# Performance work log

Measured on AMD Instinct MI355X. Metric: run time of the kernel, lower is better.

The kernel has to match this reference:

```python
import jax, jax.numpy as jnp
import numpy as np

D_MODEL = 2048
H_TOTAL = 32
D_HEAD = D_MODEL // H_TOTAL  # 64
H_ACTIVE = 4
ROPE_BASE = 10000.0


def _apply_rope(t, cos, sin):
    # t: [B, H, T, DH]; cos/sin: [T, DH//2]; interleaved pair rotation
    t1 = t[..., 0::2]
    t2 = t[..., 1::2]
    r1 = t1 * cos - t2 * sin
    r2 = t1 * sin + t2 * cos
    return jnp.stack([r1, r2], axis=-1).reshape(t.shape)


def setup_inputs() -> dict:
    key = jax.random.key(0)
    ks = jax.random.split(key, 4)
    x = jax.random.normal(ks[0], (4, 1024, D_MODEL), dtype=jnp.float32)
    w_router = jax.random.normal(ks[1], (D_MODEL, H_TOTAL), dtype=jnp.float32) * 0.02
    w_qkv = jax.random.normal(ks[2], (D_MODEL, 3 * D_MODEL), dtype=jnp.float32) * 0.02
    w_out = jax.random.normal(ks[3], (D_MODEL, D_MODEL), dtype=jnp.float32) * 0.02
    return {"x": x, "w_router": w_router, "w_qkv": w_qkv, "w_out": w_out}


def reference(x, w_router, w_qkv, w_out):
    B, T, _ = x.shape
    # --- SwitchRouter: per-token probabilities over heads ---
    probs = jax.nn.softmax(x @ w_router, axis=-1)            # [B, T, H]
    # top-h_active heads per token (dense-math equivalent of sparse dispatch)
    _, top_idx = jax.lax.top_k(probs, H_ACTIVE)              # [B, T, HA]
    mask = jnp.sum(jax.nn.one_hot(top_idx, H_TOTAL, dtype=x.dtype), axis=-2)  # [B, T, H]
    gate = probs * mask                                      # router-scored gate

    # --- QKV projection ---
    qkv = x @ w_qkv                                          # [B, T, 3D]
    q, k, v = jnp.split(qkv, 3, axis=-1)
    def to_heads(t):
        return t.reshape(B, T, H_TOTAL, D_HEAD).transpose(0, 2, 1, 3)  # [B, H, T, DH]
    q, k, v = to_heads(q), to_heads(k), to_heads(v)

    # --- RoPE ---
    inv_freq = 1.0 / (ROPE_BASE ** (jnp.arange(0, D_HEAD, 2, dtype=jnp.float32) / D_HEAD))
    ang = jnp.arange(T, dtype=jnp.float32)[:, None] * inv_freq[None, :]  # [T, DH/2]
    cos, sin = jnp.cos(ang), jnp.sin(ang)
    q = _apply_rope(q, cos, sin)
    k = _apply_rope(k, cos, sin)

    # --- causal SDPA ---
    scores = jnp.einsum('bhqd,bhkd->bhqk', q, k) / np.float32(np.sqrt(D_HEAD))
    causal = jnp.tril(jnp.ones((T, T), dtype=bool))
    scores = jnp.where(causal, scores, jnp.finfo(scores.dtype).min)
    attn = jax.nn.softmax(scores, axis=-1)
    out = jnp.einsum('bhqk,bhkd->bhqd', attn, v)             # [B, H, T, DH]

    # --- gate: only active heads contribute (scatter-back equivalent) ---
    out = out * gate.transpose(0, 2, 1)[..., None]           # [B, H, T, DH]
    out = out.transpose(0, 2, 1, 3).reshape(B, T, D_MODEL)
    return out @ w_out
```

## Files before the change

### kernel.cpp

```cpp
#include <hip/hip_runtime.h>
#include <hip/hip_bf16.h>
#include <stdint.h>
#include <stddef.h>

typedef __attribute__((ext_vector_type(8))) short bf16x8;
typedef __attribute__((ext_vector_type(8))) unsigned short u16x8;
typedef __attribute__((ext_vector_type(4))) float f32x4;
typedef __attribute__((ext_vector_type(16))) float f32x16;

#define TT 1024

__device__ __forceinline__ unsigned short f2bf(float f){
  unsigned u = __builtin_bit_cast(unsigned, f);
  unsigned r = 0x7fffu + ((u >> 16) & 1u);
  return (unsigned short)((u + r) >> 16);
}
__device__ __forceinline__ float bf2f(unsigned short s){
  unsigned u = ((unsigned)s) << 16;
  return __builtin_bit_cast(float, u);
}
__device__ __forceinline__ void gload16(const unsigned short* g, unsigned short* l){
  __builtin_amdgcn_global_load_lds(
      (const __attribute__((address_space(1))) void*)g,
      (__attribute__((address_space(3))) void*)l, 16, 0, 0);
}

__global__ void transpose_cast_kernel(const float* __restrict__ in, unsigned short* __restrict__ out,
                                      int R, int C){
  __shared__ float tile[32][33];
  int c0 = blockIdx.x * 32, r0 = blockIdx.y * 32;
  for (int i = threadIdx.y; i < 32; i += 8)
    tile[i][threadIdx.x] = in[(size_t)(r0 + i) * C + c0 + threadIdx.x];
  __syncthreads();
  for (int i = threadIdx.y; i < 32; i += 8)
    out[(size_t)(c0 + i) * R + r0 + threadIdx.x] = f2bf(tile[threadIdx.x][i]);
}

__global__ void rope_table_kernel(float* __restrict__ tab){
  int idx = blockIdx.x * 256 + threadIdx.x;
  int pos = idx >> 5, i = idx & 31;
  float freq = powf(10000.0f, -(float)i / 32.0f);
  float ang = (float)pos * freq;
  tab[idx * 2]     = cosf(ang);
  tab[idx * 2 + 1] = sinf(ang);
}

__global__ __launch_bounds__(256) void prep_kernel(const float* __restrict__ x,
                                                   const float* __restrict__ wr,
                                                   unsigned short* __restrict__ x_bf,
                                                   float* __restrict__ gate){
  __shared__ float xc[8 * 256];
  __shared__ float red[8 * 8 * 32];
  const int tid = threadIdx.x;
  const int tok0 = blockIdx.x * 8;
  const int p = tid >> 5, h = tid & 31;
  float acc[8] = {0.f,0.f,0.f,0.f,0.f,0.f,0.f,0.f};

  for (int kb = 0; kb < 8; kb++){
    __syncthreads();
    {
      int tok = tid >> 5, e = (tid & 31) * 8;
      const float* xp = x + (size_t)(tok0 + tok) * 2048 + kb * 256 + e;
      float4 v0 = *(const float4*)xp, v1 = *(const float4*)(xp + 4);
      float vals[8] = {v0.x, v0.y, v0.z, v0.w, v1.x, v1.y, v1.z, v1.w};
      u16x8 ob;
      #pragma unroll
      for (int jj = 0; jj < 8; jj++) ob[jj] = f2bf(vals[jj]);
      *(u16x8*)(x_bf + (size_t)(tok0 + tok) * 2048 + kb * 256 + e) = ob;
      #pragma unroll
      for (int jj = 0; jj < 8; jj++) xc[tok * 256 + e + jj] = vals[jj];
    }
    __syncthreads();
    const float* wp = wr + (size_t)(kb * 256 + p * 32) * 32 + h;
    #pragma unroll 4
    for (int j = 0; j < 32; j++){
      float wv = wp[j * 32];
      #pragma unroll
      for (int tok = 0; tok < 8; tok++)
        acc[tok] += xc[tok * 256 + p * 32 + j] * wv;
    }
  }
  #pragma unroll
  for (int tok = 0; tok < 8; tok++) red[(p * 8 + tok) * 32 + h] = acc[tok];
  __syncthreads();
  {
    int lane = tid & 63;
    int tok = (tid >> 6) * 2 + (lane >> 5);
    int hh = lane & 31;
    float logit = 0.f;
    #pragma unroll
    for (int pp = 0; pp < 8; pp++) logit += red[(pp * 8 + tok) * 32 + hh];
    float m = logit;
    #pragma unroll
    for (int s = 16; s >= 1; s >>= 1) m = fmaxf(m, __shfl_xor(m, s));
    float e = __expf(logit - m);
    float sum = e;
    #pragma unroll
    for (int s = 16; s >= 1; s >>= 1) sum += __shfl_xor(sum, s);
    float prob = e / sum;
    float v = logit; int sel = 0;
    #pragma unroll
    for (int rr2 = 0; rr2 < 4; rr2++){
      float bv = v; int bi = hh;
      #pragma unroll
      for (int s = 16; s >= 1; s >>= 1){
        float ov = __shfl_xor(bv, s); int oi = __shfl_xor(bi, s);
        if (ov > bv || (ov == bv && oi < bi)) { bv = ov; bi = oi; }
      }
      if (hh == bi) { sel = 1; v = -3.4e38f; }
    }
    gate[(size_t)(tok0 + tok) * 32 + hh] = sel ? prob : 0.f;
  }
}

__global__ void compact_kernel(const float* __restrict__ gate, int* __restrict__ idx,
                               int* __restrict__ counts){
  int bh = blockIdx.x;
  int b = bh >> 5, h = bh & 31;
  int lane = threadIdx.x;
  int base = 0;
  for (int c = 0; c < 16; c++){
    int t = c * 64 + lane;
    bool act = gate[(size_t)(b * TT + t) * 32 + h] != 0.f;
    unsigned long long mask = __ballot(act);
    int pos = base + __popcll(mask & ((1ull << lane) - 1ull));
    if (act) idx[bh * TT + pos] = t;
    base += __popcll(mask);
  }
  if (lane == 0) counts[bh] = base;
}

#define MFMA32(a, b, c) __builtin_amdgcn_mfma_f32_32x32x16_bf16((a), (b), (c), 0, 0, 0)

template<int EPI>
__global__ __launch_bounds__(256, 1) void gemm32(const unsigned short* __restrict__ A,
                                                 const unsigned short* __restrict__ Bt,
                                                 float* __restrict__ Cf,
                                                 unsigned short* __restrict__ qk,
                                                 unsigned short* __restrict__ vt,
                                                 const float* __restrict__ tab,
                                                 int N, int K, int nbm){
  extern __shared__ unsigned short smem[];

  const int nblk = gridDim.x;
  const int raw = blockIdx.x;
  const int tile = (raw & 7) * (nblk >> 3) + (raw >> 3);
  const int bn = tile / nbm, bm = tile % nbm;

  const int tid = threadIdx.x, lane = tid & 63, wid = tid >> 6;
  const int wrow = wid >> 1, wcol = wid & 1;
  const int l31 = lane & 31, hi = lane >> 5;
  const int X = (l31 & 7) << 4;

  const unsigned short* gA[8];
  const unsigned short* gB[4];
  #pragma unroll
  for (int p = 0; p < 8; p++){
    int L = tid * 16 + p * 4096;
    int r = L >> 7, c = (L & 127) ^ ((r & 7) << 4);
    gA[p] = A + (size_t)(bm * 256 + r) * K + (c >> 1);
  }
  #pragma unroll
  for (int p = 0; p < 4; p++){
    int L = tid * 16 + p * 4096;
    int r = L >> 7, c = (L & 127) ^ ((r & 7) << 4);
    gB[p] = Bt + (size_t)(bn * 128 + r) * K + (c >> 1);
  }

  auto stageA0 = [&](int tt){
    unsigned short* b = smem + (tt % 3) * 24576;
    size_t ko = (size_t)tt * 64;
    gload16(gA[0] + ko, b + tid * 8);
    gload16(gA[1] + ko, b + tid * 8 + 2048);
    gload16(gA[2] + ko, b + tid * 8 + 4096);
    gload16(gA[3] + ko, b + tid * 8 + 6144);
  };
  auto stageA1 = [&](int tt){
    unsigned short* b = smem + (tt % 3) * 24576;
    size_t ko = (size_t)tt * 64;
    gload16(gA[4] + ko, b + tid * 8 + 8192);
    gload16(gA[5] + ko, b + tid * 8 + 10240);
    gload16(gA[6] + ko, b + tid * 8 + 12288);
    gload16(gA[7] + ko, b + tid * 8 + 14336);
  };
  auto stageB = [&](int tt){
    unsigned short* b = smem + (tt % 3) * 24576 + 16384;
    size_t ko = (size_t)tt * 64;
    gload16(gB[0] + ko, b + tid * 8);
    gload16(gB[1] + ko, b + tid * 8 + 2048);
    gload16(gB[2] + ko, b + tid * 8 + 4096);
    gload16(gB[3] + ko, b + tid * 8 + 6144);
  };

  f32x16 acc[4][2];
  #pragma unroll
  for (int i = 0; i < 4; i++)
    #pragma unroll
    for (int j = 0; j < 2; j++) acc[i][j] = f32x16{0,0,0,0,0,0,0,0,0,0,0,0,0,0,0,0};

  const int NT = K >> 6;
  stageA0(0); stageA1(0); stageB(0);
  stageA0(1); stageA1(1); stageB(1);

  const int arow = (wrow * 128 + l31) * 64;
  const int brow = 16384 + (wcol * 64 + l31) * 64;

  for (int t = 0; t < NT; ++t){
    if (t < NT - 1) asm volatile("s_waitcnt vmcnt(12)" ::: "memory");
    else            asm volatile("s_waitcnt vmcnt(0)" ::: "memory");
    __builtin_amdgcn_s_barrier();
    __builtin_amdgcn_sched_barrier(0);
    const unsigned short* bs = smem + (t % 3) * 24576;
    const bool st = (t + 2 < NT);
    #pragma unroll
    for (int ks = 0; ks < 4; ks++){
      const int kp = ((ks * 32 + hi * 16) ^ X) >> 1;
      bf16x8 a0 = *(const bf16x8*)(bs + arow +        kp);
      bf16x8 a1 = *(const bf16x8*)(bs + arow + 2048 + kp);
      bf16x8 a2 = *(const bf16x8*)(bs + arow + 4096 + kp);
      bf16x8 a3 = *(const bf16x8*)(bs + arow + 6144 + kp);
      bf16x8 b0 = *(const bf16x8*)(bs + brow +        kp);
      bf16x8 b1 = *(const bf16x8*)(bs + brow + 2048 + kp);
      if (st && ks == 0) stageA0(t + 2);
      if (st && ks == 1) stageA1(t + 2);
      if (st && ks == 2) stageB(t + 2);
      acc[0][0] = MFMA32(a0, b0, acc[0][0]); acc[0][1] = MFMA32(a0, b1, acc[0][1]);
      acc[1][0] = MFMA32(a1, b0, acc[1][0]); acc[1][1] = MFMA32(a1, b1, acc[1][1]);
      acc[2][0] = MFMA32(a2, b0, acc[2][0]); acc[2][1] = MFMA32(a2, b1, acc[2][1]);
      acc[3][0] = MFMA32(a3, b0, acc[3][0]); acc[3][1] = MFMA32(a3, b1, acc[3][1]);
    }
  }

  if (EPI == 1){
    if (bn < 32){
      #pragma unroll
      for (int i = 0; i < 4; i++){
        #pragma unroll
        for (int j = 0; j < 2; j++){
          int col = bn * 128 + wcol * 64 + j * 32 + l31;
          int ii = (col & 63) >> 1;
          #pragma unroll
          for (int g = 0; g < 4; g++){
            #pragma unroll
            for (int rr = 0; rr < 4; rr++){
              int row = bm * 256 + wrow * 128 + i * 32 + g * 8 + hi * 4 + rr;
              int pos = row & (TT - 1);
              const float* tp = tab + ((size_t)pos * 32 + ii) * 2;
              float c = tp[0], s = tp[1];
              float val = acc[i][j][g * 4 + rr];
              float pv = __shfl_xor(val, 1);
              float res = (lane & 1) ? (pv * s + val * c) : (val * c - pv * s);
              qk[(size_t)row * 4096 + col] = f2bf(res);
            }
          }
        }
      }
    } else {
      #pragma unroll
      for (int i = 0; i < 4; i++){
        #pragma unroll
        for (int j = 0; j < 2; j++){
          int vcol = bn * 128 + wcol * 64 + j * 32 + l31 - 4096;
          int hh = vcol >> 6, d = vcol & 63;
          int row0 = bm * 256 + wrow * 128 + i * 32 + hi * 4;
          int b = row0 >> 10, t0 = row0 & (TT - 1);
          #pragma unroll
          for (int g = 0; g < 4; g++){
            ushort4 pk;
            pk.x = f2bf(acc[i][j][g * 4 + 0]); pk.y = f2bf(acc[i][j][g * 4 + 1]);
            pk.z = f2bf(acc[i][j][g * 4 + 2]); pk.w = f2bf(acc[i][j][g * 4 + 3]);
            *(ushort4*)(vt + ((size_t)((b * 32 + hh) * 64 + d)) * TT + t0 + g * 8) = pk;
          }
        }
      }
    }
  } else {
    #pragma unroll
    for (int i = 0; i < 4; i++){
      #pragma unroll
      for (int j = 0; j < 2; j++){
        int col = bn * 128 + wcol * 64 + j * 32 + l31;
        #pragma unroll
        for (int g = 0; g < 4; g++){
          #pragma unroll
          for (int rr = 0; rr < 4; rr++){
            size_t row = (size_t)(bm * 256 + wrow * 128 + i * 32 + g * 8 + hi * 4 + rr);
            Cf[row * N + col] = acc[i][j][g * 4 + rr];
          }
        }
      }
    }
  }
}

#define MFMA_B16(a, b, c) __builtin_amdgcn_mfma_f32_16x16x32_bf16((a), (b), (c), 0, 0, 0)
__global__ __launch_bounds__(256) void attn_sparse_kernel(const unsigned short* __restrict__ qk,
                                                          const unsigned short* __restrict__ vt,
                                                          const float* __restrict__ gate,
                                                          const int* __restrict__ idx,
                                                          const int* __restrict__ counts,
                                                          unsigned short* __restrict__ attn_out){
  __shared__ unsigned short Ks[64 * 64];
  __shared__ unsigned short Vs[64 * 64];
  __shared__ unsigned short Ps[4][16 * 64];
  const int bh = blockIdx.x, qt = blockIdx.y;
  const int count = counts[bh];
  if (qt * 64 >= count) return;
  const int b = bh >> 5, h = bh & 31;
  const int tid = threadIdx.x, lane = tid & 63, w = tid >> 6;
  const int li = lane & 15, lg = lane >> 4;
  const int* myidx = idx + bh * TT + qt * 64;
  const int nvalid = min(64, count - qt * 64);
  const int qmax = myidx[nvalid - 1];

  int qi[4];
  #pragma unroll
  for (int r = 0; r < 4; r++){
    int s = w * 16 + lg * 4 + r;
    qi[r] = (s < nvalid) ? myidx[s] : -1;
  }
  int qrow = (w * 16 + li < nvalid) ? myidx[w * 16 + li] : 0;
  bf16x8 qf0, qf1;
  {
    const unsigned short* qp = qk + (size_t)(b * TT + qrow) * 4096 + h * 64;
    qf0 = *(const bf16x8*)(qp + lg * 8);
    qf1 = *(const bf16x8*)(qp + 32 + lg * 8);
  }
  f32x4 o[4];
  #pragma unroll
  for (int i = 0; i < 4; i++) o[i] = f32x4{0.f, 0.f, 0.f, 0.f};
  float m_run[4], l_run[4];
  #pragma unroll
  for (int r = 0; r < 4; r++){ m_run[r] = -1e30f; l_run[r] = 0.f; }

  const int nkt = (qmax >> 6) + 1;
  for (int kt = 0; kt < nkt; kt++){
    const int kb = kt * 64;
    #pragma unroll
    for (int s2 = 0; s2 < 2; s2++){
      int s = s2 * 256 + tid;
      int r = s >> 3, c = (s & 7) * 8;
      gload16(qk + (size_t)(b * TT + kb + r) * 4096 + 2048 + h * 64 + c, &Ks[s * 8]);
      gload16(vt + (size_t)(bh * 64 + r) * TT + kb + c, &Vs[s * 8]);
    }
    __syncthreads();

    f32x4 s4[4];
    #pragma unroll
    for (int ni = 0; ni < 4; ni++){
      bf16x8 k0 = *(const bf16x8*)(&Ks[(ni * 16 + li) * 64 + lg * 8]);
      bf16x8 k1 = *(const bf16x8*)(&Ks[(ni * 16 + li) * 64 + 32 + lg * 8]);
      f32x4 t = f32x4{0.f, 0.f, 0.f, 0.f};
      t = MFMA_B16(qf0, k0, t);
      t = MFMA_B16(qf1, k1, t);
      s4[ni] = t;
    }
    float mt[4];
    #pragma unroll
    for (int r = 0; r < 4; r++) mt[r] = -1e30f;
    #pragma unroll
    for (int ni = 0; ni < 4; ni++){
      int kidx = kb + ni * 16 + li;
      #pragma unroll
      for (int r = 0; r < 4; r++){
        float val = s4[ni][r] * 0.125f;
        val = (kidx <= qi[r]) ? val : -1e30f;
        s4[ni][r] = val;
        mt[r] = fmaxf(mt[r], val);
      }
    }
    #pragma unroll
    for (int r = 0; r < 4; r++){
      #pragma unroll
      for (int sh = 8; sh >= 1; sh >>= 1) mt[r] = fmaxf(mt[r], __shfl_xor(mt[r], sh));
      float mnew = fmaxf(m_run[r], mt[r]);
      float corr = __expf(m_run[r] - mnew);
      m_run[r] = mnew;
      l_run[r] *= corr;
      #pragma unroll
      for (int j = 0; j < 4; j++) o[j][r] *= corr;
    }
    float rs[4] = {0.f, 0.f, 0.f, 0.f};
    #pragma unroll
    for (int ni = 0; ni < 4; ni++)
      #pragma unroll
      for (int r = 0; r < 4; r++){
        float p = __expf(s4[ni][r] - m_run[r]);
        s4[ni][r] = p;
        rs[r] += p;
      }
    #pragma unroll
    for (int r = 0; r < 4; r++){
      #pragma unroll
      for (int sh = 8; sh >= 1; sh >>= 1) rs[r] += __shfl_xor(rs[r], sh);
      l_run[r] += rs[r];
    }
    #pragma unroll
    for (int ni = 0; ni < 4; ni++)
      #pragma unroll
      for (int r = 0; r < 4; r++)
        Ps[w][(lg * 4 + r) * 64 + ni * 16 + li] = f2bf(s4[ni][r]);
    #pragma unroll
    for (int ks = 0; ks < 2; ks++){
      bf16x8 pa = *(const bf16x8*)(&Ps[w][li * 64 + ks * 32 + lg * 8]);
      #pragma unroll
      for (int ni = 0; ni < 4; ni++){
        bf16x8 vb = *(const bf16x8*)(&Vs[(ni * 16 + li) * 64 + ks * 32 + lg * 8]);
        o[ni] = MFMA_B16(pa, vb, o[ni]);
      }
    }
    __syncthreads();
  }
  #pragma unroll
  for (int r = 0; r < 4; r++){
    if (qi[r] < 0) continue;
    float g = gate[(size_t)(b * TT + qi[r]) * 32 + h];
    float inv = g / l_run[r];
    #pragma unroll
    for (int ni = 0; ni < 4; ni++)
      attn_out[(size_t)(b * TT + qi[r]) * 2048 + h * 64 + ni * 16 + li] = f2bf(o[ni][r] * inv);
  }
}

extern "C" void kernel_launch(void* const* d_in, const int* in_sizes, int n_in,
                              void* d_out, int out_size, void* d_ws, size_t ws_size,
                              hipStream_t stream){
  const float* x        = (const float*)d_in[0];
  const float* w_router = (const float*)d_in[1];
  const float* w_qkv    = (const float*)d_in[2];
  const float* w_out    = (const float*)d_in[3];
  float* out = (float*)d_out;
  char* ws = (char*)d_ws;

  unsigned short* qk    = (unsigned short*)(ws);
  unsigned short* vt    = (unsigned short*)(ws + 33554432);
  unsigned short* x_bf  = (unsigned short*)(ws + 50331648);
  unsigned short* wqkvT = (unsigned short*)(ws + 67108864);
  unsigned short* woutT = (unsigned short*)(ws + 92274688);
  float* gate           = (float*)(ws + 100663296);
  float* tab            = (float*)(ws + 101187584);
  unsigned short* attn  = x_bf;
  int* idx              = (int*)(ws + 67108864);
  int* counts           = (int*)(ws + 67633152);

  constexpr int GEMM_LDS = 147456;
  (void)hipFuncSetAttribute(reinterpret_cast<const void*>(&gemm32<1>),
                            hipFuncAttributeMaxDynamicSharedMemorySize, GEMM_LDS);
  (void)hipFuncSetAttribute(reinterpret_cast<const void*>(&gemm32<0>),
                            hipFuncAttributeMaxDynamicSharedMemorySize, GEMM_LDS);

  hipLaunchKernelGGL(transpose_cast_kernel, dim3(192, 64), dim3(32, 8), 0, stream, w_qkv, wqkvT, 2048, 6144);
  hipLaunchKernelGGL(transpose_cast_kernel, dim3(64, 64), dim3(32, 8), 0, stream, w_out, woutT, 2048, 2048);
  hipLaunchKernelGGL(rope_table_kernel, dim3(128), dim3(256), 0, stream, tab);
  hipLaunchKernelGGL(prep_kernel, dim3(512), dim3(256), 0, stream, x, w_router, x_bf, gate);
  hipLaunchKernelGGL((gemm32<1>), dim3(768), dim3(256), GEMM_LDS, stream,
                     x_bf, wqkvT, (float*)nullptr, qk, vt, tab, 6144, 2048, 16);
  hipLaunchKernelGGL(compact_kernel, dim3(128), dim3(64), 0, stream, gate, idx, counts);
  (void)hipMemsetAsync(attn, 0, (size_t)4096 * 2048 * 2, stream);
  hipLaunchKernelGGL(attn_sparse_kernel, dim3(128, 16), dim3(256), 0, stream, qk, vt, gate, idx, counts, attn);
  hipLaunchKernelGGL((gemm32<0>), dim3(256), dim3(256), GEMM_LDS, stream,
                     attn, woutT, out, (unsigned short*)nullptr, (unsigned short*)nullptr,
                     (const float*)nullptr, 2048, 2048, 16);
}
```

Baseline: 270.1 us.

## Compute Q projection only for router-selected token-head pairs via sparse gather GEMM

The dense QKV GEMM now produces only K and V (4096 columns). A new gathered qgemm_kernel computes Q only for the top-4 active heads of each token, with RoPE applied in its epilogue. To support this, prep_kernel emits per-token head lists and compact_kernel runs before the GEMM, storing a slot index alongside each token. This cuts the dense GEMM work by a third, since only 4 of 32 heads need Q. The cost is a gather-based GEMM with uncoalesced row loads that has no LDS staging and splits K across waves with an LDS reduction.

```diff
diff --git a/kernel.cpp b/kernel.cpp
--- a/kernel.cpp
+++ b/kernel.cpp
@@ -24,6 +24,9 @@
       (const __attribute__((address_space(1))) void*)g,
       (__attribute__((address_space(3))) void*)l, 16, 0, 0);
 }
+
+#define MFMA32(a, b, c) __builtin_amdgcn_mfma_f32_32x32x16_bf16((a), (b), (c), 0, 0, 0)
+#define MFMA_B16(a, b, c) __builtin_amdgcn_mfma_f32_16x16x32_bf16((a), (b), (c), 0, 0, 0)
 
 __global__ void transpose_cast_kernel(const float* __restrict__ in, unsigned short* __restrict__ out,
                                       int R, int C){
@@ -48,7 +51,8 @@
 __global__ __launch_bounds__(256) void prep_kernel(const float* __restrict__ x,
                                                    const float* __restrict__ wr,
                                                    unsigned short* __restrict__ x_bf,
-                                                   float* __restrict__ gate){
+                                                   float* __restrict__ gate,
+                                                   unsigned char* __restrict__ heads4){
   __shared__ float xc[8 * 256];
   __shared__ float red[8 * 8 * 32];
   const int tid = threadIdx.x;
@@ -110,38 +114,121 @@
       if (hh == bi) { sel = 1; v = -3.4e38f; }
     }
     gate[(size_t)(tok0 + tok) * 32 + hh] = sel ? prob : 0.f;
-  }
-}
-
-__global__ void compact_kernel(const float* __restrict__ gate, int* __restrict__ idx,
-                               int* __restrict__ counts){
+    unsigned long long bal = __ballot(sel != 0);
+    unsigned selmask = (unsigned)(bal >> ((lane >> 5) * 32));
+    if (sel){
+      int r = __popc(selmask & ((1u << hh) - 1u));
+      heads4[(size_t)(tok0 + tok) * 4 + r] = (unsigned char)hh;
+    }
+  }
+}
+
+__global__ void compact_kernel(const unsigned char* __restrict__ heads4,
+                               unsigned short* __restrict__ idx, int* __restrict__ counts){
   int bh = blockIdx.x;
   int b = bh >> 5, h = bh & 31;
   int lane = threadIdx.x;
   int base = 0;
   for (int c = 0; c < 16; c++){
     int t = c * 64 + lane;
-    bool act = gate[(size_t)(b * TT + t) * 32 + h] != 0.f;
+    unsigned u = ((const unsigned*)heads4)[b * 1024 + t];
+    int r = -1;
+    if (((u      ) & 255) == (unsigned)h) r = 0;
+    else if (((u >>  8) & 255) == (unsigned)h) r = 1;
+    else if (((u >> 16) & 255) == (unsigned)h) r = 2;
+    else if (((u >> 24) & 255) == (unsigned)h) r = 3;
+    bool act = (r >= 0);
     unsigned long long mask = __ballot(act);
     int pos = base + __popcll(mask & ((1ull << lane) - 1ull));
-    if (act) idx[bh * TT + pos] = t;
+    if (act) idx[bh * 1024 + pos] = (unsigned short)(t | (r << 10));
     base += __popcll(mask);
   }
   if (lane == 0) counts[bh] = base;
 }
 
-#define MFMA32(a, b, c) __builtin_amdgcn_mfma_f32_32x32x16_bf16((a), (b), (c), 0, 0, 0)
+__global__ __launch_bounds__(256) void qgemm_kernel(const unsigned short* __restrict__ x_bf,
+                                                    const unsigned short* __restrict__ wqkvT,
+                                                    const unsigned short* __restrict__ idx,
+                                                    const int* __restrict__ counts,
+                                                    const float* __restrict__ tab,
+                                                    unsigned short* __restrict__ qact){
+  __shared__ float red[4][64][64];
+  const int bh = blockIdx.x, qt = blockIdx.y;
+  const int count = counts[bh];
+  if (qt * 64 >= count) return;
+  const int b = bh >> 5, h = bh & 31;
+  const int tid = threadIdx.x, lane = tid & 63, w = tid >> 6;
+  const int li = lane & 15, lg = lane >> 4;
+  const int nvalid = min(64, count - qt * 64);
+  const unsigned short* myidx = idx + bh * 1024 + qt * 64;
+
+  int atok[4];
+  #pragma unroll
+  for (int ai = 0; ai < 4; ai++){
+    int s = ai * 16 + li;
+    atok[ai] = (s < nvalid) ? (myidx[s] & 1023) : 0;
+  }
+  const unsigned short* Bbase = wqkvT + (size_t)(h * 64) * 2048;
+
+  f32x4 acc[4][4];
+  #pragma unroll
+  for (int i = 0; i < 4; i++)
+    #pragma unroll
+    for (int j = 0; j < 4; j++) acc[i][j] = f32x4{0.f, 0.f, 0.f, 0.f};
+
+  const int k0w = w * 512;
+  #pragma unroll 2
+  for (int ks = 0; ks < 16; ks++){
+    int k0 = k0w + ks * 32 + lg * 8;
+    bf16x8 af[4], bw[4];
+    #pragma unroll
+    for (int ai = 0; ai < 4; ai++)
+      af[ai] = *(const bf16x8*)(x_bf + (size_t)(b * 1024 + atok[ai]) * 2048 + k0);
+    #pragma unroll
+    for (int ni = 0; ni < 4; ni++)
+      bw[ni] = *(const bf16x8*)(Bbase + (size_t)(ni * 16 + li) * 2048 + k0);
+    #pragma unroll
+    for (int ai = 0; ai < 4; ai++)
+      #pragma unroll
+      for (int ni = 0; ni < 4; ni++)
+        acc[ai][ni] = MFMA_B16(af[ai], bw[ni], acc[ai][ni]);
+  }
+  #pragma unroll
+  for (int ai = 0; ai < 4; ai++)
+    #pragma unroll
+    for (int ni = 0; ni < 4; ni++)
+      #pragma unroll
+      for (int rr = 0; rr < 4; rr++)
+        red[w][ai * 16 + lg * 4 + rr][ni * 16 + li] = acc[ai][ni][rr];
+  __syncthreads();
+
+  int q = tid >> 2, dbase = (tid & 3) * 16;
+  if (q < nvalid){
+    int e = myidx[q];
+    int tok = e & 1023, r = e >> 10;
+    unsigned short* op = qact + ((size_t)((b << 10) + tok) * 4 + r) * 64;
+    const float* tp = tab + ((size_t)tok * 32 + (dbase >> 1)) * 2;
+    #pragma unroll
+    for (int p = 0; p < 8; p++){
+      int d0 = dbase + 2 * p;
+      float v0 = red[0][q][d0] + red[1][q][d0] + red[2][q][d0] + red[3][q][d0];
+      float v1 = red[0][q][d0 + 1] + red[1][q][d0 + 1] + red[2][q][d0 + 1] + red[3][q][d0 + 1];
+      float c = tp[2 * p], s = tp[2 * p + 1];
+      op[d0]     = f2bf(v0 * c - v1 * s);
+      op[d0 + 1] = f2bf(v0 * s + v1 * c);
+    }
+  }
+}
 
 template<int EPI>
 __global__ __launch_bounds__(256, 1) void gemm32(const unsigned short* __restrict__ A,
                                                  const unsigned short* __restrict__ Bt,
                                                  float* __restrict__ Cf,
-                                                 unsigned short* __restrict__ qk,
+                                                 unsigned short* __restrict__ kbuf,
                                                  unsigned short* __restrict__ vt,
                                                  const float* __restrict__ tab,
                                                  int N, int K, int nbm){
   extern __shared__ unsigned short smem[];
-
   const int nblk = gridDim.x;
   const int raw = blockIdx.x;
   const int tile = (raw & 7) * (nblk >> 3) + (raw >> 3);
@@ -232,7 +319,7 @@
   }
 
   if (EPI == 1){
-    if (bn < 32){
+    if (bn < 16){
       #pragma unroll
       for (int i = 0; i < 4; i++){
         #pragma unroll
@@ -250,7 +337,7 @@
               float val = acc[i][j][g * 4 + rr];
               float pv = __shfl_xor(val, 1);
               float res = (lane & 1) ? (pv * s + val * c) : (val * c - pv * s);
-              qk[(size_t)row * 4096 + col] = f2bf(res);
+              kbuf[(size_t)row * 2048 + col] = f2bf(res);
             }
           }
         }
@@ -260,7 +347,7 @@
       for (int i = 0; i < 4; i++){
         #pragma unroll
         for (int j = 0; j < 2; j++){
-          int vcol = bn * 128 + wcol * 64 + j * 32 + l31 - 4096;
+          int vcol = bn * 128 + wcol * 64 + j * 32 + l31 - 2048;
           int hh = vcol >> 6, d = vcol & 63;
           int row0 = bm * 256 + wrow * 128 + i * 32 + hi * 4;
           int b = row0 >> 10, t0 = row0 & (TT - 1);
@@ -293,11 +380,11 @@
   }
 }
 
-#define MFMA_B16(a, b, c) __builtin_amdgcn_mfma_f32_16x16x32_bf16((a), (b), (c), 0, 0, 0)
-__global__ __launch_bounds__(256) void attn_sparse_kernel(const unsigned short* __restrict__ qk,
+__global__ __launch_bounds__(256) void attn_sparse_kernel(const unsigned short* __restrict__ qact,
+                                                          const unsigned short* __restrict__ kbuf,
                                                           const unsigned short* __restrict__ vt,
                                                           const float* __restrict__ gate,
-                                                          const int* __restrict__ idx,
+                                                          const unsigned short* __restrict__ idx,
                                                           const int* __restrict__ counts,
                                                           unsigned short* __restrict__ attn_out){
   __shared__ unsigned short Ks[64 * 64];
@@ -309,20 +396,21 @@
   const int b = bh >> 5, h = bh & 31;
   const int tid = threadIdx.x, lane = tid & 63, w = tid >> 6;
   const int li = lane & 15, lg = lane >> 4;
-  const int* myidx = idx + bh * TT + qt * 64;
+  const unsigned short* myidx = idx + bh * 1024 + qt * 64;
   const int nvalid = min(64, count - qt * 64);
-  const int qmax = myidx[nvalid - 1];
+  const int qmax = myidx[nvalid - 1] & 1023;
 
   int qi[4];
   #pragma unroll
   for (int r = 0; r < 4; r++){
     int s = w * 16 + lg * 4 + r;
-    qi[r] = (s < nvalid) ? myidx[s] : -1;
-  }
-  int qrow = (w * 16 + li < nvalid) ? myidx[w * 16 + li] : 0;
+    qi[r] = (s < nvalid) ? (myidx[s] & 1023) : -1;
+  }
   bf16x8 qf0, qf1;
   {
-    const unsigned short* qp = qk + (size_t)(b * TT + qrow) * 4096 + h * 64;
+    int s = w * 16 + li;
+    int e2 = (s < nvalid) ? myidx[s] : 0;
+    const unsigned short* qp = qact + ((size_t)((b << 10) + (e2 & 1023)) * 4 + (e2 >> 10)) * 64;
     qf0 = *(const bf16x8*)(qp + lg * 8);
     qf1 = *(const bf16x8*)(qp + 32 + lg * 8);
   }
@@ -340,7 +428,7 @@
     for (int s2 = 0; s2 < 2; s2++){
       int s = s2 * 256 + tid;
       int r = s >> 3, c = (s & 7) * 8;
-      gload16(qk + (size_t)(b * TT + kb + r) * 4096 + 2048 + h * 64 + c, &Ks[s * 8]);
+      gload16(kbuf + (size_t)(b * TT + kb + r) * 2048 + h * 64 + c, &Ks[s * 8]);
       gload16(vt + (size_t)(bh * 64 + r) * TT + kb + c, &Vs[s * 8]);
     }
     __syncthreads();
@@ -432,16 +520,18 @@
   float* out = (float*)d_out;
   char* ws = (char*)d_ws;
 
-  unsigned short* qk    = (unsigned short*)(ws);
-  unsigned short* vt    = (unsigned short*)(ws + 33554432);
-  unsigned short* x_bf  = (unsigned short*)(ws + 50331648);
-  unsigned short* wqkvT = (unsigned short*)(ws + 67108864);
-  unsigned short* woutT = (unsigned short*)(ws + 92274688);
-  float* gate           = (float*)(ws + 100663296);
-  float* tab            = (float*)(ws + 101187584);
-  unsigned short* attn  = x_bf;
-  int* idx              = (int*)(ws + 67108864);
-  int* counts           = (int*)(ws + 67633152);
+  unsigned short* kbuf   = (unsigned short*)(ws);
+  unsigned short* vt     = (unsigned short*)(ws + 16777216);
+  unsigned short* qact   = (unsigned short*)(ws + 33554432);
+  unsigned short* idx    = (unsigned short*)(ws + 37748736);
+  int* counts            = (int*)(ws + 38010880);
+  unsigned char* heads4  = (unsigned char*)(ws + 38011392);
+  unsigned short* x_bf   = (unsigned short*)(ws + 50331648);
+  unsigned short* wqkvT  = (unsigned short*)(ws + 67108864);
+  unsigned short* woutT  = (unsigned short*)(ws + 92274688);
+  float* gate            = (float*)(ws + 100663296);
+  float* tab             = (float*)(ws + 101187584);
+  unsigned short* attn   = x_bf;
 
   constexpr int GEMM_LDS = 147456;
   (void)hipFuncSetAttribute(reinterpret_cast<const void*>(&gemm32<1>),
@@ -452,12 +542,15 @@
   hipLaunchKernelGGL(transpose_cast_kernel, dim3(192, 64), dim3(32, 8), 0, stream, w_qkv, wqkvT, 2048, 6144);
   hipLaunchKernelGGL(transpose_cast_kernel, dim3(64, 64), dim3(32, 8), 0, stream, w_out, woutT, 2048, 2048);
   hipLaunchKernelGGL(rope_table_kernel, dim3(128), dim3(256), 0, stream, tab);
-  hipLaunchKernelGGL(prep_kernel, dim3(512), dim3(256), 0, stream, x, w_router, x_bf, gate);
-  hipLaunchKernelGGL((gemm32<1>), dim3(768), dim3(256), GEMM_LDS, stream,
-                     x_bf, wqkvT, (float*)nullptr, qk, vt, tab, 6144, 2048, 16);
-  hipLaunchKernelGGL(compact_kernel, dim3(128), dim3(64), 0, stream, gate, idx, counts);
+  hipLaunchKernelGGL(prep_kernel, dim3(512), dim3(256), 0, stream, x, w_router, x_bf, gate, heads4);
+  hipLaunchKernelGGL(compact_kernel, dim3(128), dim3(64), 0, stream, heads4, idx, counts);
+  hipLaunchKernelGGL((gemm32<1>), dim3(512), dim3(256), GEMM_LDS, stream,
+                     x_bf, wqkvT + (size_t)2048 * 2048, (float*)nullptr, kbuf, vt, tab, 4096, 2048, 16);
+  hipLaunchKernelGGL(qgemm_kernel, dim3(128, 16), dim3(256), 0, stream,
+                     x_bf, wqkvT, idx, counts, tab, qact);
   (void)hipMemsetAsync(attn, 0, (size_t)4096 * 2048 * 2, stream);
-  hipLaunchKernelGGL(attn_sparse_kernel, dim3(128, 16), dim3(256), 0, stream, qk, vt, gate, idx, counts, attn);
+  hipLaunchKernelGGL(attn_sparse_kernel, dim3(128, 16), dim3(256), 0, stream,
+                     qact, kbuf, vt, gate, idx, counts, attn);
   hipLaunchKernelGGL((gemm32<0>), dim3(256), dim3(256), GEMM_LDS, stream,
                      attn, woutT, out, (unsigned short*)nullptr, (unsigned short*)nullptr,
                      (const float*)nullptr, 2048, 2048, 16);
```

After: 263.5 us. 2.4% less time.
